# Kernel tuning notes

Hardware: AMD Instinct MI355X
Metric: run time of the kernel (lower is better)

The kernel has to match this reference:

```python
import jax, jax.numpy as jnp
import numpy as np

BN_EPS = 1e-5
# regular 3x3 kernel grid offsets: row0 = dy, row1 = dx, kernel positions in row-major order
REG = jnp.array([[-1, -1, -1, 0, 0, 0, 1, 1, 1],
                 [-1,  0,  1, -1, 0, 1, -1, 0, 1]], dtype=jnp.float32)


def conv3x3(x, w, b):
    y = jax.lax.conv_general_dilated(x, w, window_strides=(1, 1),
                                     padding=((1, 1), (1, 1)),
                                     dimension_numbers=('NCHW', 'OIHW', 'NCHW'))
    return y + b[None, :, None, None]


def deform_conv3x3(x, dy, dx, w):
    # x: [N,C,H,W]; dy,dx: [N,9,H,W] per-kernel-tap offsets; w: [O,C,3,3]
    N, C, H, W = x.shape
    K = 9
    ky = jnp.repeat(jnp.arange(3), 3)   # [0,0,0,1,1,1,2,2,2]
    kx = jnp.tile(jnp.arange(3), 3)     # [0,1,2,0,1,2,0,1,2]
    # sampling positions: p = p_out - pad + k*dilation + offset (stride=1, pad=dil=1)
    py = dy + (jnp.arange(H) - 1)[None, None, :, None] + ky[None, :, None, None].astype(x.dtype)
    px = dx + (jnp.arange(W) - 1)[None, None, None, :] + kx[None, :, None, None].astype(x.dtype)
    y0 = jnp.floor(py)
    x0 = jnp.floor(px)
    wy = py - y0  # bilinear weights
    wx = px - x0
    y0i = y0.astype(jnp.int32)
    x0i = x0.astype(jnp.int32)
    nidx = jnp.arange(N)[:, None, None, None]

    def gather(yi, xi):
        valid = ((yi >= 0) & (yi < H) & (xi >= 0) & (xi < W)).astype(x.dtype)
        v = x[nidx, :, jnp.clip(yi, 0, H - 1), jnp.clip(xi, 0, W - 1)]  # [N,K,H,W,C]
        return v * valid[..., None]

    sampled = (gather(y0i,     x0i)     * ((1 - wy) * (1 - wx))[..., None]
             + gather(y0i,     x0i + 1) * ((1 - wy) * wx)[..., None]
             + gather(y0i + 1, x0i)     * (wy * (1 - wx))[..., None]
             + gather(y0i + 1, x0i + 1) * (wy * wx)[..., None])  # [N,K,H,W,C]
    O = w.shape[0]
    return jnp.einsum('nkhwc,ock->nohw', sampled, w.reshape(O, C, K))


def setup_inputs() -> dict:
    key = jax.random.key(0)
    ks = jax.random.split(key, 12)
    N, C, H, W = 2, 256, 96, 96
    O = 256
    sc = 1.0 / np.sqrt(C * 9)
    return {
        'x': jax.random.normal(ks[0], (N, C, H, W), jnp.float32),
        'mask_attention': jax.random.normal(ks[1], (N, C, H, W), jnp.float32),
        'w_tm': jax.random.normal(ks[2], (4, C, 3, 3), jnp.float32) * sc,
        'b_tm': jax.random.normal(ks[3], (4,), jnp.float32) * 0.01,
        'w_tr': jax.random.normal(ks[4], (2, C, 3, 3), jnp.float32) * sc,
        'b_tr': jax.random.normal(ks[5], (2,), jnp.float32) * 0.01,
        'w_deform': jax.random.normal(ks[6], (O, C, 3, 3), jnp.float32) * sc,
        'bn_gamma': jnp.ones((O,), jnp.float32),
        'bn_beta': jnp.zeros((O,), jnp.float32),
        'bn_mean': jax.random.normal(ks[7], (O,), jnp.float32) * 0.01,
        'bn_var': jax.random.uniform(ks[8], (O,), jnp.float32, 0.5, 1.5),
    }


def reference(x, mask_attention, w_tm, b_tm, w_tr, b_tr, w_deform,
              bn_gamma, bn_beta, bn_mean, bn_var):
    # mask_attention is overwritten by x in the original forward; ignored.
    N, C, H, W = x.shape
    tm = conv3x3(x, w_tm, b_tm)                       # [N,4,H,W]
    T = tm.transpose(0, 2, 3, 1).reshape(N, H, W, 2, 2)
    off = jnp.einsum('nhwij,jk->nhwik', T, REG) - REG  # [N,H,W,2,9], (T-I)@REG
    tr = conv3x3(x, w_tr, b_tr)                        # [N,2,H,W]
    off = off + tr.transpose(0, 2, 3, 1)[..., None]    # broadcast translation to all 9 taps
    dy = off[..., 0, :].transpose(0, 3, 1, 2)          # [N,9,H,W]
    dx = off[..., 1, :].transpose(0, 3, 1, 2)
    out = deform_conv3x3(x, dy, dx, w_deform)          # [N,O,H,W]
    inv = jax.lax.rsqrt(bn_var + BN_EPS)
    out = (out - bn_mean[None, :, None, None]) * (inv * bn_gamma)[None, :, None, None] \
          + bn_beta[None, :, None, None]
    return jax.nn.relu(out + x)
```

## Files before the change

kernel.cpp:

```cpp
#include <hip/hip_runtime.h>
#include <stdint.h>

#define H_ 96
#define W_ 96
#define C_ 256
#define O_ 256
#define N_ 2
#define HW_ (H_*W_)
#define M_ (N_*HW_)
#define GK 2304

typedef _Float16 f16x8 __attribute__((ext_vector_type(8)));
typedef _Float16 f16x2 __attribute__((ext_vector_type(2)));
typedef float f32x4 __attribute__((ext_vector_type(4)));
typedef unsigned short us4 __attribute__((ext_vector_type(4)));
typedef unsigned short us8 __attribute__((ext_vector_type(8)));

__device__ __forceinline__ unsigned short f2h(float f) {
  union { _Float16 h; unsigned short u; } v;
  v.h = (_Float16)f;
  return v.u;
}
__device__ __forceinline__ f16x2 hpair(float f) {
  const _Float16 h = (_Float16)f;
  return (f16x2){h, h};
}

__global__ __launch_bounds__(256) void k_pre(const float* __restrict__ x,
                                             const float* __restrict__ w_df,
                                             const float* __restrict__ w_tm,
                                             const float* __restrict__ w_tr,
                                             unsigned short* __restrict__ xt,
                                             unsigned short* __restrict__ wfrag,
                                             unsigned short* __restrict__ w6p) {
  const int b = blockIdx.x;
  const int tid = threadIdx.x;
  if (b < 576) {
    __shared__ unsigned short tile[64][130];
    const int pt = b % 144;
    const int ch = (b / 144) & 1;
    const int n  = b / 288;
    const int p0 = pt * 64, c0 = ch * 128;
    const float* xp = x + (size_t)n * C_ * HW_;
    unsigned short* xtp = xt + (size_t)n * C_ * HW_;
    const int tx = tid & 15, ty = tid >> 4;
#pragma unroll
    for (int pass = 0; pass < 8; pass++) {
      const int c = pass * 16 + ty;
      const f32x4 v = *(const f32x4*)(xp + (size_t)(c0 + c) * HW_ + p0 + tx * 4);
#pragma unroll
      for (int i = 0; i < 4; i++) tile[tx * 4 + i][c] = f2h(v[i]);
    }
    __syncthreads();
    const int l32 = tid & 31, pr = tid >> 5;
#pragma unroll
    for (int pass = 0; pass < 8; pass++) {
      const int p = pass * 8 + pr;
      us4 v;
#pragma unroll
      for (int i = 0; i < 4; i++) v[i] = tile[p][l32 * 4 + i];
      *(us4*)(xtp + (size_t)(p0 + p) * C_ + c0 + l32 * 4) = v;
    }
  } else if (b < 864) {
    const int base = (b - 576) * 2048 + tid * 8;
    const int l  = (base >> 3) & 63;
    const int g  = (base >> 9) & 15;
    const int ks = (base >> 13) & 7;
    const int t  = base >> 16;
    const int o  = g * 16 + (l & 15);
    const int c  = ks * 32 + (l >> 4) * 8;
    us8 res;
#pragma unroll
    for (int j = 0; j < 8; j++) res[j] = f2h(w_df[(size_t)(o * 256 + c + j) * 9 + t]);
    *(us8*)(wfrag + base) = res;
  } else {
    int idx = (b - 864) * 256 + tid;
    int t = idx >> 12;
    int r = idx & 4095;
    int j = r >> 8;
    int c = r & 255;
    float v = 0.f;
    if (j < 4) v = w_tm[(size_t)(j * C_ + c) * 9 + t];
    else if (j < 6) v = w_tr[(size_t)((j - 4) * C_ + c) * 9 + t];
    w6p[idx] = f2h(v);
  }
}

__global__ __launch_bounds__(512, 2) void k_fused(const unsigned short* __restrict__ xt,
                                                  const unsigned short* __restrict__ Wfrag,
                                                  const unsigned short* __restrict__ w6p,
                                                  const float* __restrict__ b_tm,
                                                  const float* __restrict__ b_tr,
                                                  const float* __restrict__ xres,
                                                  const float* __restrict__ gamma,
                                                  const float* __restrict__ beta,
                                                  const float* __restrict__ mean,
                                                  const float* __restrict__ var,
                                                  float* __restrict__ out) {
  __shared__ unsigned short As[2][80 * 256] __attribute__((aligned(16)));
  __shared__ float sred5[5][8][16][8];
  __shared__ float coords_s[80][9][2];
  __shared__ int   nofs[80];
  const int tid = threadIdx.x;
  const int wave = tid >> 6, lane = tid & 63;
  const int row = lane & 15, quad = lane >> 4;
  const int pb = (blockIdx.x & 7) * 32 + (blockIdx.x >> 3);
  const bool fat = pb < 128;
  const int nt = fat ? 5 : 4;
  const int m0 = fat ? pb * 80 : 10240 + (pb - 128) * 64;
  const int sr = tid >> 4;
  const int cg = tid & 15;

#pragma unroll
  for (int t5 = 0; t5 < 5; ++t5) {
    if (t5 < nt) {
      const int ts = m0 + t5 * 16;
      const int nn = ts / HW_;
      const int hw = ts - nn * HW_;
      const int h = hw / W_, w0 = hw - h * W_;
      const unsigned short* xts = xt + (size_t)nn * C_ * HW_;
      const int cq = wave * 32;
      f32x4 oacc = {0.f, 0.f, 0.f, 0.f};
      const f16x8 zero8 = {};
#pragma unroll
      for (int t = 0; t < 9; t++) {
        const int ty = t / 3, tx = t % 3;
        const int y = h + ty - 1;
        if (y < 0 || y >= H_) continue;
        const int xx = w0 + row + tx - 1;
        const bool valid = (xx >= 0) && (xx < W_);
        const int xc = min(max(xx, 0), W_ - 1);
        f16x8 av = *(const f16x8*)(const void*)(xts + (size_t)(y * W_ + xc) * C_ + cq + quad * 8);
        if (!valid) av = zero8;
        const f16x8 bv = *(const f16x8*)(const void*)(w6p + (size_t)(t * 16 + row) * C_ + cq + quad * 8);
        oacc = __builtin_amdgcn_mfma_f32_16x16x32_f16(av, bv, oacc, 0, 0, 0);
      }
      if (row < 6) {
#pragma unroll
        for (int r = 0; r < 4; r++) sred5[t5][wave][quad * 4 + r][row] = oacc[r];
      }
    }
  }
  __syncthreads();
  if (tid < nt * 16) {
    const int rg = tid;
    const int gm = m0 + rg;
    const int nn = gm / HW_;
    const int hw = gm - nn * HW_;
    const int h = hw / W_, w = hw - h * W_;
    const int tt = rg >> 4, mm = rg & 15;
    float a[6];
#pragma unroll
    for (int j = 0; j < 6; j++) {
      float s = 0.f;
#pragma unroll
      for (int wv = 0; wv < 8; wv++) s += sred5[tt][wv][mm][j];
      a[j] = s;
    }
    const float tm0 = a[0] + b_tm[0];
    const float tm1 = a[1] + b_tm[1];
    const float tm2 = a[2] + b_tm[2];
    const float tm3 = a[3] + b_tm[3];
    const float tr0 = a[4] + b_tr[0];
    const float tr1 = a[5] + b_tr[1];
#pragma unroll
    for (int t = 0; t < 9; t++) {
      const float ry = (float)(t / 3) - 1.f;
      const float rx = (float)(t % 3) - 1.f;
      coords_s[rg][t][0] = (float)h + tr0 + tm0 * ry + tm1 * rx;
      coords_s[rg][t][1] = (float)w + tr1 + tm2 * ry + tm3 * rx;
    }
    nofs[rg] = nn * (C_ * HW_);
  }
  __syncthreads();

  f32x4 acc[5][2] = {};
  f16x2 cwh0, cwh1, cwh2, cwh3;
  int cb[4];
  us8 u0[4], u1[4];

#define STAGEROW(R, TAP, ASB)                                                  \
  {                                                                            \
    const int r_ = (R);                                                        \
    const int nof = nofs[r_];                                                  \
    const float py = coords_s[r_][TAP][0];                                     \
    const float px = coords_s[r_][TAP][1];                                     \
    const float fy = floorf(py), fx = floorf(px);                              \
    const float wy = py - fy, wx = px - fx;                                    \
    const int y0 = (int)fy, x0 = (int)fx;                                      \
    const int y1 = y0 + 1, x1 = x0 + 1;                                        \
    const float vy0 = (y0 >= 0 && y0 < H_) ? 1.f : 0.f;                        \
    const float vy1 = (y1 >= 0 && y1 < H_) ? 1.f : 0.f;                        \
    const float vx0 = (x0 >= 0 && x0 < W_) ? 1.f : 0.f;                        \
    const float vx1 = (x1 >= 0 && x1 < W_) ? 1.f : 0.f;                        \
    cwh0 = hpair((1.f - wy) * (1.f - wx) * vy0 * vx0);                         \
    cwh1 = hpair((1.f - wy) * wx * vy0 * vx1);                                 \
    cwh2 = hpair(wy * (1.f - wx) * vy1 * vx0);                                 \
    cwh3 = hpair(wy * wx * vy1 * vx1);                                         \
    const int cy0 = min(max(y0, 0), H_ - 1), cy1 = min(max(y1, 0), H_ - 1);    \
    const int cx0 = min(max(x0, 0), W_ - 1), cx1 = min(max(x1, 0), W_ - 1);    \
    cb[0] = nof + (cy0 * W_ + cx0) * C_;                                       \
    cb[1] = nof + (cy0 * W_ + cx1) * C_;                                       \
    cb[2] = nof + (cy1 * W_ + cx0) * C_;                                       \
    cb[3] = nof + (cy1 * W_ + cx1) * C_;                                       \
    const int cc = cg * 16;                                                    \
    u0[0] = *(const us8*)(xt + cb[0] + cc); u1[0] = *(const us8*)(xt + cb[0] + cc + 8); \
    u0[1] = *(const us8*)(xt + cb[1] + cc); u1[1] = *(const us8*)(xt + cb[1] + cc + 8); \
    u0[2] = *(const us8*)(xt + cb[2] + cc); u1[2] = *(const us8*)(xt + cb[2] + cc + 8); \
    u0[3] = *(const us8*)(xt + cb[3] + cc); u1[3] = *(const us8*)(xt + cb[3] + cc + 8); \
    us8 r0v, r1v;                                                              \
    {                                                                          \
      const f16x2* p0 = (const f16x2*)&u0[0];                                  \
      const f16x2* p1 = (const f16x2*)&u0[1];                                  \
      const f16x2* p2 = (const f16x2*)&u0[2];                                  \
      const f16x2* p3 = (const f16x2*)&u0[3];                                  \
      f16x2* d = (f16x2*)&r0v;                                                 \
      _Pragma("unroll")                                                        \
      for (int p = 0; p < 4; p++) {                                            \
        f16x2 r = p0[p] * cwh0; r = p1[p] * cwh1 + r;                          \
        r = p2[p] * cwh2 + r;   r = p3[p] * cwh3 + r;  d[p] = r;               \
      }                                                                        \
    }                                                                          \
    {                                                                          \
      const f16x2* p0 = (const f16x2*)&u1[0];                                  \
      const f16x2* p1 = (const f16x2*)&u1[1];                                  \
      const f16x2* p2 = (const f16x2*)&u1[2];                                  \
      const f16x2* p3 = (const f16x2*)&u1[3];                                  \
      f16x2* d = (f16x2*)&r1v;                                                 \
      _Pragma("unroll")                                                        \
      for (int p = 0; p < 4; p++) {                                            \
        f16x2 r = p0[p] * cwh0; r = p1[p] * cwh1 + r;                          \
        r = p2[p] * cwh2 + r;   r = p3[p] * cwh3 + r;  d[p] = r;               \
      }                                                                        \
    }                                                                          \
    const int q0i = cg * 2, q1i = cg * 2 + 1;                                  \
    const int s0 = (q0i & 24) | ((q0i ^ r_) & 7);                              \
    const int s1 = (q1i & 24) | ((q1i ^ r_) & 7);                              \
    *(us8*)(void*)&ASB[r_ * 256 + s0 * 8] = r0v;                               \
    *(us8*)(void*)&ASB[r_ * 256 + s1 * 8] = r1v;                               \
  }

  for (int tap = 0; tap < 9; tap++) {
    unsigned short* __restrict__ asb = &As[tap & 1][0];

    STAGEROW(sr, tap, asb);
    STAGEROW(sr + 32, tap, asb);
    if (fat) {
      if (sr < 16) STAGEROW(sr + 64, tap, asb);
    }

    const unsigned short* wfTap =
        Wfrag + (size_t)tap * 65536 + wave * 1024 + lane * 8;
    f16x8 bv[2];
#pragma unroll
    for (int ot = 0; ot < 2; ot++) bv[ot] = *(const f16x8*)(const void*)(wfTap + ot * 512);
    __builtin_amdgcn_sched_barrier(0);

    __syncthreads();

#pragma unroll
    for (int ks = 0; ks < 8; ks++) {
      const int q = ks * 4 + quad;
      const int slot = (q & 24) | ((q ^ row) & 7);
      f16x8 a0 = *(const f16x8*)(const void*)&asb[(0 * 16 + row) * 256 + slot * 8];
      f16x8 a1 = *(const f16x8*)(const void*)&asb[(1 * 16 + row) * 256 + slot * 8];
      f16x8 a2 = *(const f16x8*)(const void*)&asb[(2 * 16 + row) * 256 + slot * 8];
      f16x8 a3 = *(const f16x8*)(const void*)&asb[(3 * 16 + row) * 256 + slot * 8];
      f16x8 a4;
      if (fat) a4 = *(const f16x8*)(const void*)&asb[(4 * 16 + row) * 256 + slot * 8];
      f16x8 bn[2];
      if (ks < 7) {
        const unsigned short* wfn = wfTap + (size_t)(ks + 1) * 8192;
#pragma unroll
        for (int ot = 0; ot < 2; ot++) bn[ot] = *(const f16x8*)(const void*)(wfn + ot * 512);
      }
#pragma unroll
      for (int ot = 0; ot < 2; ot++) {
        acc[0][ot] = __builtin_amdgcn_mfma_f32_16x16x32_f16(a0, bv[ot], acc[0][ot], 0, 0, 0);
        acc[1][ot] = __builtin_amdgcn_mfma_f32_16x16x32_f16(a1, bv[ot], acc[1][ot], 0, 0, 0);
        acc[2][ot] = __builtin_amdgcn_mfma_f32_16x16x32_f16(a2, bv[ot], acc[2][ot], 0, 0, 0);
        acc[3][ot] = __builtin_amdgcn_mfma_f32_16x16x32_f16(a3, bv[ot], acc[3][ot], 0, 0, 0);
      }
      if (fat) {
#pragma unroll
        for (int ot = 0; ot < 2; ot++)
          acc[4][ot] = __builtin_amdgcn_mfma_f32_16x16x32_f16(a4, bv[ot], acc[4][ot], 0, 0, 0);
      }
      if (ks < 7) {
#pragma unroll
        for (int ot = 0; ot < 2; ot++) bv[ot] = bn[ot];
      }
    }
  }

#pragma unroll
  for (int ot = 0; ot < 2; ot++) {
    const int o = wave * 32 + ot * 16 + row;
    const float sc = rsqrtf(var[o] + 1e-5f) * gamma[o];
    const float bi = beta[o] - mean[o] * sc;
#pragma unroll
    for (int t5 = 0; t5 < 5; t5++) {
      if (t5 < nt) {
        const int ts = m0 + t5 * 16;
        const int nn = ts / HW_;
        const int hw0 = ts - nn * HW_ + quad * 4;
        const size_t ob = (size_t)(nn * O_ + o) * HW_ + hw0;
        const f32x4 rv = *(const f32x4*)(xres + ob);
        f32x4 ov;
#pragma unroll
        for (int r = 0; r < 4; r++) ov[r] = fmaxf(acc[t5][ot][r] * sc + bi + rv[r], 0.f);
        *(f32x4*)(out + ob) = ov;
      }
    }
  }
}

extern "C" void kernel_launch(void* const* d_in, const int* in_sizes, int n_in,
                              void* d_out, int out_size, void* d_ws, size_t ws_size,
                              hipStream_t stream) {
  const float* x     = (const float*)d_in[0];
  const float* w_tm  = (const float*)d_in[2];
  const float* b_tm  = (const float*)d_in[3];
  const float* w_tr  = (const float*)d_in[4];
  const float* b_tr  = (const float*)d_in[5];
  const float* w_df  = (const float*)d_in[6];
  const float* gamma = (const float*)d_in[7];
  const float* beta  = (const float*)d_in[8];
  const float* mean  = (const float*)d_in[9];
  const float* var   = (const float*)d_in[10];
  float* out = (float*)d_out;

  char* ws = (char*)d_ws;
  unsigned short* xt    = (unsigned short*)(ws);
  unsigned short* wfrag = (unsigned short*)(ws + 9437184);
  unsigned short* w6p   = (unsigned short*)(ws + 9437184 + 1179648);

  k_pre<<<1008, 256, 0, stream>>>(x, w_df, w_tm, w_tr, xt, wfrag, w6p);
  k_fused<<<256, 512, 0, stream>>>(xt, wfrag, w6p, b_tm, b_tr, x,
                                   gamma, beta, mean, var, out);
}
```

Baseline: 162.3 us.

## Software-pipeline deformable gather loads across taps with double register buffers

Splits the per-row staging into an issue phase (coordinate math plus global gathers into registers) and a lerp/write phase, using two register buffer sets. The first row's gathers for the next tap are issued before the MFMA loop of the current tap, and the second row's gathers go out before the first row's lerp, so gather latency overlaps compute. The cost is more live vector registers, which could lower occupancy or cause spills.

```diff
diff --git a/kernel.cpp b/kernel.cpp
--- a/kernel.cpp
+++ b/kernel.cpp
@@ -175,11 +175,10 @@
   __syncthreads();
 
   f32x4 acc[5][2] = {};
-  f16x2 cwh0, cwh1, cwh2, cwh3;
-  int cb[4];
-  us8 u0[4], u1[4];
-
-#define STAGEROW(R, TAP, ASB)                                                  \
+  float cwA[4], cwB[4];
+  us8 uA0[4], uA1[4], uB0[4], uB1[4];
+
+#define ISSUE(S, R, TAP)                                                       \
   {                                                                            \
     const int r_ = (R);                                                        \
     const int nof = nofs[r_];                                                  \
@@ -193,44 +192,50 @@
     const float vy1 = (y1 >= 0 && y1 < H_) ? 1.f : 0.f;                        \
     const float vx0 = (x0 >= 0 && x0 < W_) ? 1.f : 0.f;                        \
     const float vx1 = (x1 >= 0 && x1 < W_) ? 1.f : 0.f;                        \
-    cwh0 = hpair((1.f - wy) * (1.f - wx) * vy0 * vx0);                         \
-    cwh1 = hpair((1.f - wy) * wx * vy0 * vx1);                                 \
-    cwh2 = hpair(wy * (1.f - wx) * vy1 * vx0);                                 \
-    cwh3 = hpair(wy * wx * vy1 * vx1);                                         \
+    cw##S[0] = (1.f - wy) * (1.f - wx) * vy0 * vx0;                            \
+    cw##S[1] = (1.f - wy) * wx * vy0 * vx1;                                    \
+    cw##S[2] = wy * (1.f - wx) * vy1 * vx0;                                    \
+    cw##S[3] = wy * wx * vy1 * vx1;                                            \
     const int cy0 = min(max(y0, 0), H_ - 1), cy1 = min(max(y1, 0), H_ - 1);    \
     const int cx0 = min(max(x0, 0), W_ - 1), cx1 = min(max(x1, 0), W_ - 1);    \
-    cb[0] = nof + (cy0 * W_ + cx0) * C_;                                       \
-    cb[1] = nof + (cy0 * W_ + cx1) * C_;                                       \
-    cb[2] = nof + (cy1 * W_ + cx0) * C_;                                       \
-    cb[3] = nof + (cy1 * W_ + cx1) * C_;                                       \
-    const int cc = cg * 16;                                                    \
-    u0[0] = *(const us8*)(xt + cb[0] + cc); u1[0] = *(const us8*)(xt + cb[0] + cc + 8); \
-    u0[1] = *(const us8*)(xt + cb[1] + cc); u1[1] = *(const us8*)(xt + cb[1] + cc + 8); \
-    u0[2] = *(const us8*)(xt + cb[2] + cc); u1[2] = *(const us8*)(xt + cb[2] + cc + 8); \
-    u0[3] = *(const us8*)(xt + cb[3] + cc); u1[3] = *(const us8*)(xt + cb[3] + cc + 8); \
+    const int b0 = nof + (cy0 * W_ + cx0) * C_ + cg * 16;                      \
+    const int b1 = nof + (cy0 * W_ + cx1) * C_ + cg * 16;                      \
+    const int b2 = nof + (cy1 * W_ + cx0) * C_ + cg * 16;                      \
+    const int b3 = nof + (cy1 * W_ + cx1) * C_ + cg * 16;                      \
+    u##S##0[0] = *(const us8*)(xt + b0); u##S##1[0] = *(const us8*)(xt + b0 + 8); \
+    u##S##0[1] = *(const us8*)(xt + b1); u##S##1[1] = *(const us8*)(xt + b1 + 8); \
+    u##S##0[2] = *(const us8*)(xt + b2); u##S##1[2] = *(const us8*)(xt + b2 + 8); \
+    u##S##0[3] = *(const us8*)(xt + b3); u##S##1[3] = *(const us8*)(xt + b3 + 8); \
+  }
+
+#define LERPW(S, R, ASB)                                                       \
+  {                                                                            \
+    const int r_ = (R);                                                        \
+    const f16x2 c0 = hpair(cw##S[0]), c1 = hpair(cw##S[1]);                    \
+    const f16x2 c2 = hpair(cw##S[2]), c3 = hpair(cw##S[3]);                    \
     us8 r0v, r1v;                                                              \
     {                                                                          \
-      const f16x2* p0 = (const f16x2*)&u0[0];                                  \
-      const f16x2* p1 = (const f16x2*)&u0[1];                                  \
-      const f16x2* p2 = (const f16x2*)&u0[2];                                  \
-      const f16x2* p3 = (const f16x2*)&u0[3];                                  \
+      const f16x2* p0 = (const f16x2*)&u##S##0[0];                             \
+      const f16x2* p1 = (const f16x2*)&u##S##0[1];                             \
+      const f16x2* p2 = (const f16x2*)&u##S##0[2];                             \
+      const f16x2* p3 = (const f16x2*)&u##S##0[3];                             \
       f16x2* d = (f16x2*)&r0v;                                                 \
       _Pragma("unroll")                                                        \
       for (int p = 0; p < 4; p++) {                                            \
-        f16x2 r = p0[p] * cwh0; r = p1[p] * cwh1 + r;                          \
-        r = p2[p] * cwh2 + r;   r = p3[p] * cwh3 + r;  d[p] = r;               \
+        f16x2 r = p0[p] * c0; r = p1[p] * c1 + r;                              \
+        r = p2[p] * c2 + r;   r = p3[p] * c3 + r;  d[p] = r;                   \
       }                                                                        \
     }                                                                          \
     {                                                                          \
-      const f16x2* p0 = (const f16x2*)&u1[0];                                  \
-      const f16x2* p1 = (const f16x2*)&u1[1];                                  \
-      const f16x2* p2 = (const f16x2*)&u1[2];                                  \
-      const f16x2* p3 = (const f16x2*)&u1[3];                                  \
+      const f16x2* p0 = (const f16x2*)&u##S##1[0];                             \
+      const f16x2* p1 = (const f16x2*)&u##S##1[1];                             \
+      const f16x2* p2 = (const f16x2*)&u##S##1[2];                             \
+      const f16x2* p3 = (const f16x2*)&u##S##1[3];                             \
       f16x2* d = (f16x2*)&r1v;                                                 \
       _Pragma("unroll")                                                        \
       for (int p = 0; p < 4; p++) {                                            \
-        f16x2 r = p0[p] * cwh0; r = p1[p] * cwh1 + r;                          \
-        r = p2[p] * cwh2 + r;   r = p3[p] * cwh3 + r;  d[p] = r;               \
+        f16x2 r = p0[p] * c0; r = p1[p] * c1 + r;                              \
+        r = p2[p] * c2 + r;   r = p3[p] * c3 + r;  d[p] = r;                   \
       }                                                                        \
     }                                                                          \
     const int q0i = cg * 2, q1i = cg * 2 + 1;                                  \
@@ -240,15 +245,15 @@
     *(us8*)(void*)&ASB[r_ * 256 + s1 * 8] = r1v;                               \
   }
 
+  const bool third = fat && (sr < 16);
+
+  ISSUE(A, sr, 0);
+  __builtin_amdgcn_sched_barrier(0);
+
   for (int tap = 0; tap < 9; tap++) {
     unsigned short* __restrict__ asb = &As[tap & 1][0];
 
-    STAGEROW(sr, tap, asb);
-    STAGEROW(sr + 32, tap, asb);
-    if (fat) {
-      if (sr < 16) STAGEROW(sr + 64, tap, asb);
-    }
-
+    ISSUE(B, sr + 32, tap);
     const unsigned short* wfTap =
         Wfrag + (size_t)tap * 65536 + wave * 1024 + lane * 8;
     f16x8 bv[2];
@@ -256,7 +261,20 @@
     for (int ot = 0; ot < 2; ot++) bv[ot] = *(const f16x8*)(const void*)(wfTap + ot * 512);
     __builtin_amdgcn_sched_barrier(0);
 
+    LERPW(A, sr, asb);
+    if (third) {
+      ISSUE(A, sr + 64, tap);
+      __builtin_amdgcn_sched_barrier(0);
+    }
+    LERPW(B, sr + 32, asb);
+    if (third) LERPW(A, sr + 64, asb);
+
     __syncthreads();
+
+    if (tap < 8) {
+      ISSUE(A, sr, tap + 1);
+      __builtin_amdgcn_sched_barrier(0);
+    }
 
 #pragma unroll
     for (int ks = 0; ks < 8; ks++) {
```

Measured after the change: 165.7 us. 2.1% more time.
